# Optimization experiments

Measured on AMD Instinct MI355X. Metric: run time of the kernel, lower is better.

The kernel has to match this reference:

```python
import jax, jax.numpy as jnp
import numpy as np
from jax import lax

B, D, E, H, W = 256, 64, 16, 64, 64
PROJ, FC, NA = 512, 1024, 2

def _conv(x, w, pad):
    # x: [N,C,H,W], w: [O,I,kh,kw]
    return lax.conv_general_dilated(x, w, (1, 1), [(pad, pad), (pad, pad)],
                                    dimension_numbers=('NCHW', 'OIHW', 'NCHW'))

def _maxpool2(x):
    return lax.reduce_window(x, -jnp.inf, lax.max, (1, 1, 2, 2), (1, 1, 2, 2), 'VALID')

def _sample_conv(x, w, b):
    # per-sample conv with its own gathered expert weights: x [D,h,w], w [D,D,3,3]
    y = lax.conv_general_dilated(x[None], w, (1, 1), [(1, 1), (1, 1)],
                                 dimension_numbers=('NCHW', 'OIHW', 'NCHW'))[0]
    return y + b[:, None, None]

_expert_conv = jax.vmap(_sample_conv)  # batch of samples, each with its own kernel

def setup_inputs() -> dict:
    key = jax.random.key(0)
    ks = jax.random.split(key, 12)
    s = 0.05
    return {
        'image': jax.random.normal(ks[0], (B, 3, H, W), jnp.float32),
        'question': jax.random.randint(ks[1], (B, 8), 0, E),
        'stem_w0': jax.random.normal(ks[2], (D, 3, 3, 3), jnp.float32) * s,
        'stem_b0': jnp.zeros((D,), jnp.float32),
        'stem_w': jax.random.normal(ks[3], (3, D, D, 3, 3), jnp.float32) * s,
        'stem_b': jnp.zeros((3, D), jnp.float32),
        'exp_w1': jax.random.normal(ks[4], (E, D, D, 3, 3), jnp.float32) * s,
        'exp_b1': jnp.zeros((E, D), jnp.float32),
        'exp_w2': jax.random.normal(ks[5], (E, D, D, 3, 3), jnp.float32) * s,
        'exp_b2': jnp.zeros((E, D), jnp.float32),
        'proj_w': jax.random.normal(ks[6], (PROJ, D, 1, 1), jnp.float32) * s,
        'proj_b': jnp.zeros((PROJ,), jnp.float32),
        'fc1_w': jax.random.normal(ks[7], (FC, PROJ * 8 * 8), jnp.float32) * 0.01,
        'fc1_b': jnp.zeros((FC,), jnp.float32),
        'fc2_w': jax.random.normal(ks[8], (NA, FC), jnp.float32) * 0.01,
        'fc2_b': jnp.zeros((NA,), jnp.float32),
    }

def reference(image, question, stem_w0, stem_b0, stem_w, stem_b,
              exp_w1, exp_b1, exp_w2, exp_b2,
              proj_w, proj_b, fc1_w, fc1_b, fc2_w, fc2_b):
    # --- stem: 4 conv3x3 + ReLU, maxpool after layers 0 and 2 (64->32->16) ---
    h = jax.nn.relu(_conv(image, stem_w0, 1) + stem_b0[None, :, None, None])
    h = _maxpool2(h)
    h = jax.nn.relu(_conv(h, stem_w[0], 1) + stem_b[0][None, :, None, None])
    h = jax.nn.relu(_conv(h, stem_w[1], 1) + stem_b[1][None, :, None, None])
    h = _maxpool2(h)
    h = jax.nn.relu(_conv(h, stem_w[2], 1) + stem_b[2][None, :, None, None])
    # --- chain1 routing: cols (lhs=4, rel=5, rhs=7) each pick a ResidualBlock expert ---
    for col in (4, 5, 7):
        idx = question[:, col]                       # [B] expert ids
        w1, b1 = exp_w1[idx], exp_b1[idx]            # gather per-sample kernels
        w2, b2 = exp_w2[idx], exp_b2[idx]
        mid = jax.nn.relu(_expert_conv(h, w1, b1))   # conv1 + ReLU
        out = _expert_conv(mid, w2, b2)              # conv2 (no BN)
        h = jax.nn.relu(h + out)                     # residual + ReLU
    # --- classifier: 1x1 proj + ReLU, maxpool2, flatten, fc, fc ---
    c = jax.nn.relu(_conv(h, proj_w, 0) + proj_b[None, :, None, None])  # [B,512,16,16]
    c = _maxpool2(c)                                                     # [B,512,8,8]
    c = c.reshape(c.shape[0], -1)                                        # [B,32768]
    c = jax.nn.relu(c @ fc1_w.T + fc1_b)
    return c @ fc2_w.T + fc2_b                                           # [B,2]
```

## Files before the change

### kernel.cpp

```cpp
#include <hip/hip_runtime.h>
#include <cstddef>


typedef _Float16 half8 __attribute__((ext_vector_type(8)));
typedef _Float16 half4_t __attribute__((ext_vector_type(4)));
typedef float f32x4 __attribute__((ext_vector_type(4)));

#define LO_SCALE 2048.0f
#define LO_INV (1.0f / 2048.0f)

__global__ void transw_k(const float* __restrict__ src, float* __restrict__ dst,
                         int O, int I, int K, int total) {
    int id = blockIdx.x * 256 + threadIdx.x;
    if (id >= total) return;
    int OIK = O * I * K;
    int n = id / OIK, rem = id % OIK;
    int o = rem / (I * K), r2 = rem % (I * K);
    int i = r2 / K, k = r2 % K;
    dst[(size_t)n * OIK + (i * K + k) * O + o] = src[id];
}

__global__ void wxform_k(const float* __restrict__ src, _Float16* __restrict__ dst,
                         int nlayers) {
    int id = blockIdx.x * 256 + threadIdx.x;
    if (id >= nlayers * 36864) return;
    int layer = id / 36864, idx = id % 36864;
    int j = idx & 7, l = (idx >> 3) & 63, nt = (idx >> 9) & 3;
    int icc = (idx >> 11) & 1, tap = idx >> 12;
    int kl = (l >> 4) * 8 + j, ic = icc * 32 + kl, oc = nt * 16 + (l & 15);
    float v = src[(size_t)layer * 36864 + (oc * 64 + ic) * 9 + tap];
    _Float16 hi = (_Float16)v;
    _Float16 lo = (_Float16)((v - (float)hi) * LO_SCALE);
    dst[(size_t)layer * 73728 + idx] = hi;
    dst[(size_t)layer * 73728 + 36864 + idx] = lo;
}

__global__ void pwxform_k(const float* __restrict__ src, _Float16* __restrict__ dst) {
    int id = blockIdx.x * 256 + threadIdx.x;
    if (id >= 32768) return;
    int j = id & 7, l = (id >> 3) & 63, icc = (id >> 9) & 1, nt = id >> 10;
    int kl = (l >> 4) * 8 + j, ic = icc * 32 + kl, oc = nt * 16 + (l & 15);
    float v = src[oc * 64 + ic];
    _Float16 hi = (_Float16)v;
    _Float16 lo = (_Float16)((v - (float)hi) * LO_SCALE);
    dst[id] = hi;
    dst[32768 + id] = lo;
}

__global__ __launch_bounds__(256)
void conv1_k(const float* __restrict__ img, const float* __restrict__ w0t,
             const float* __restrict__ b0, float* __restrict__ out) {
    int b = blockIdx.x, tile = blockIdx.y, ocg = blockIdx.z;
    int typ = (tile >> 1) * 16, txp = (tile & 1) * 16;
    int cy0 = typ * 2, cx0 = txp * 2;
    __shared__ float lds[3][34][34];
    const float* imb = img + (size_t)b * 3 * 64 * 64;
    for (int i = threadIdx.x; i < 3 * 34 * 34; i += 256) {
        int c = i / 1156, rem = i % 1156, r = rem / 34, cc = rem % 34;
        int gy = cy0 - 1 + r, gx = cx0 - 1 + cc;
        float v = 0.f;
        if (gy >= 0 && gy < 64 && gx >= 0 && gx < 64) v = imb[(c * 64 + gy) * 64 + gx];
        lds[c][r][cc] = v;
    }
    __syncthreads();
    int pyl = threadIdx.x >> 4, pxl = threadIdx.x & 15;
    float win[3][4][4];
#pragma unroll
    for (int c = 0; c < 3; ++c)
#pragma unroll
        for (int wy = 0; wy < 4; ++wy)
#pragma unroll
            for (int wx = 0; wx < 4; ++wx)
                win[c][wy][wx] = lds[c][2 * pyl + wy][2 * pxl + wx];
    int py = typ + pyl, px = txp + pxl;
    float* op = &out[(((size_t)b * 32 + py) * 32 + px) * 64];
#pragma unroll
    for (int q = 0; q < 4; ++q) {
        int ocq = ocg * 4 + q;
        float acc[4][4] = {};
#pragma unroll
        for (int c = 0; c < 3; ++c)
#pragma unroll
            for (int ky = 0; ky < 3; ++ky)
#pragma unroll
                for (int kx = 0; kx < 3; ++kx) {
                    float4 w = *(const float4*)&w0t[(c * 9 + ky * 3 + kx) * 64 + ocq * 4];
                    float wv4[4] = {w.x, w.y, w.z, w.w};
#pragma unroll
                    for (int p2 = 0; p2 < 4; ++p2) {
                        float iv = win[c][(p2 >> 1) + ky][(p2 & 1) + kx];
#pragma unroll
                        for (int o = 0; o < 4; ++o)
                            acc[p2][o] = fmaf(iv, wv4[o], acc[p2][o]);
                    }
                }
        float4 res;
        float* rp = (float*)&res;
#pragma unroll
        for (int o = 0; o < 4; ++o) {
            float bvv = b0[ocq * 4 + o];
            float m = fmaxf(fmaxf(acc[0][o], acc[1][o]), fmaxf(acc[2][o], acc[3][o]));
            rp[o] = fmaxf(m + bvv, 0.f);
        }
        *(float4*)&op[ocq * 4] = res;
    }
}

template <int S, bool POOL, bool RES>
__global__ __launch_bounds__(256, 2)
void convm_k(const float* __restrict__ in, float* __restrict__ out,
             const _Float16* __restrict__ wf, const float* __restrict__ bias,
             const float* __restrict__ res, const int* __restrict__ question,
             int qcol) {
    int b = blockIdx.x, t = blockIdx.y;
    constexpr int NTX = S / 16;
    int ty0 = (t / NTX) * 8, tx0 = (t % NTX) * 16;

    __shared__ __align__(16) _Float16 lds[2 * 7200];

    int tid = threadIdx.x, lane = tid & 63, wv = tid >> 6;
    const _Float16* wb = wf;
    const float* bb = bias;
    if (question) {
        int idx = question[b * 8 + qcol];
        wb += (size_t)idx * 73728;
        bb += idx * 64;
    }
    float bv[4];
#pragma unroll
    for (int nt = 0; nt < 4; ++nt) bv[nt] = bb[nt * 16 + (lane & 15)];

    f32x4 acc1[2][4] = {};
    f32x4 acc2[2][4] = {};

    int am = lane & 15;
    int k0 = (lane >> 4) * 8;

    for (int icc = 0; icc < 2; ++icc) {
        __syncthreads();
        for (int i = tid; i < 1440; i += 256) {
            int pix = i >> 3, j4 = i & 7;
            int hy = pix / 18, hx = pix % 18;
            int gy = ty0 + hy - 1, gx = tx0 + hx - 1;
            float4 v = {0.f, 0.f, 0.f, 0.f};
            if (gy >= 0 && gy < S && gx >= 0 && gx < S)
                v = *(const float4*)&in[(((size_t)b * S + gy) * S + gx) * 64 + icc * 32 + j4 * 4];
            _Float16 h0 = (_Float16)v.x, h1 = (_Float16)v.y;
            _Float16 h2 = (_Float16)v.z, h3 = (_Float16)v.w;
            half4_t hh = {h0, h1, h2, h3};
            half4_t ll = {(_Float16)((v.x - (float)h0) * LO_SCALE),
                          (_Float16)((v.y - (float)h1) * LO_SCALE),
                          (_Float16)((v.z - (float)h2) * LO_SCALE),
                          (_Float16)((v.w - (float)h3) * LO_SCALE)};
            *(half4_t*)&lds[pix * 40 + j4 * 4] = hh;
            *(half4_t*)&lds[7200 + pix * 40 + j4 * 4] = ll;
        }
        __syncthreads();

#pragma unroll
        for (int ky = 0; ky < 3; ++ky)
#pragma unroll
            for (int kx = 0; kx < 3; ++kx) {
                int tap = ky * 3 + kx;
                const _Float16* wp = wb + (tap * 2 + icc) * 2048 + lane * 8;
                half8 bhi[4], blo[4];
#pragma unroll
                for (int nt = 0; nt < 4; ++nt) {
                    bhi[nt] = *(const half8*)(wp + nt * 512);
                    blo[nt] = *(const half8*)(wp + nt * 512 + 36864);
                }
#pragma unroll
                for (int mt = 0; mt < 2; ++mt) {
                    int MT = wv * 2 + mt;
                    int Q = MT * 4 + (am >> 2), s = am & 3;
                    int py = (Q >> 3) * 2 + (s >> 1), px = (Q & 7) * 2 + (s & 1);
                    const _Float16* ap = &lds[((py + ky) * 18 + (px + kx)) * 40 + k0];
                    half8 ahi = *(const half8*)ap;
                    half8 alo = *(const half8*)(ap + 7200);
#pragma unroll
                    for (int nt = 0; nt < 4; ++nt) {
                        acc1[mt][nt] = __builtin_amdgcn_mfma_f32_16x16x32_f16(
                            ahi, bhi[nt], acc1[mt][nt], 0, 0, 0);
                        acc2[mt][nt] = __builtin_amdgcn_mfma_f32_16x16x32_f16(
                            ahi, blo[nt], acc2[mt][nt], 0, 0, 0);
                        acc2[mt][nt] = __builtin_amdgcn_mfma_f32_16x16x32_f16(
                            alo, bhi[nt], acc2[mt][nt], 0, 0, 0);
                    }
                }
            }
    }

    int cn = lane & 15, rq = lane >> 4;
#pragma unroll
    for (int mt = 0; mt < 2; ++mt) {
        int MT = wv * 2 + mt;
        int Q = MT * 4 + rq;
        int qy = Q >> 3, qx = Q & 7;
#pragma unroll
        for (int nt = 0; nt < 4; ++nt) {
            int oc = nt * 16 + cn;
            float vals[4];
#pragma unroll
            for (int r = 0; r < 4; ++r)
                vals[r] = acc1[mt][nt][r] + acc2[mt][nt][r] * LO_INV + bv[nt];
            if (POOL) {
                float m = fmaxf(fmaxf(vals[0], vals[1]), fmaxf(vals[2], vals[3]));
                m = fmaxf(m, 0.f);
                int opy = (ty0 >> 1) + qy, opx = (tx0 >> 1) + qx;
                out[(((size_t)b * (S / 2) + opy) * (S / 2) + opx) * 64 + oc] = m;
            } else {
#pragma unroll
                for (int r = 0; r < 4; ++r) {
                    int py = qy * 2 + (r >> 1), px = qx * 2 + (r & 1);
                    size_t o = (((size_t)b * S + (ty0 + py)) * S + (tx0 + px)) * 64 + oc;
                    float v = vals[r];
                    if (RES) v += res[o];
                    out[o] = fmaxf(v, 0.f);
                }
            }
        }
    }
}

__global__ __launch_bounds__(256)
void projm_k(const float* __restrict__ in ,
             const _Float16* __restrict__ pw, const float* __restrict__ bias,
             float* __restrict__ out ) {
    int b = blockIdx.x;
    __shared__ float lt[64 * 65];
    int tid = threadIdx.x, lane = tid & 63, wv = tid >> 6;
    int row = lane & 15, cseg = lane >> 4;

    half8 ah[4][2], al[4][2];
#pragma unroll
    for (int mt = 0; mt < 4; ++mt) {
        int MT = wv * 4 + mt;
        int Q = MT * 4 + (row >> 2), s = row & 3;
        int y = (Q >> 3) * 2 + (s >> 1), x = (Q & 7) * 2 + (s & 1);
        const float* ip = in + ((size_t)b * 256 + y * 16 + x) * 64 + cseg * 8;
#pragma unroll
        for (int icc = 0; icc < 2; ++icc) {
            float4 v0 = *(const float4*)(ip + icc * 32);
            float4 v1 = *(const float4*)(ip + icc * 32 + 4);
            _Float16 h0 = (_Float16)v0.x, h1 = (_Float16)v0.y;
            _Float16 h2 = (_Float16)v0.z, h3 = (_Float16)v0.w;
            _Float16 h4 = (_Float16)v1.x, h5 = (_Float16)v1.y;
            _Float16 h6 = (_Float16)v1.z, h7 = (_Float16)v1.w;
            ah[mt][icc] = (half8){h0, h1, h2, h3, h4, h5, h6, h7};
            al[mt][icc] = (half8){(_Float16)((v0.x - (float)h0) * LO_SCALE),
                                  (_Float16)((v0.y - (float)h1) * LO_SCALE),
                                  (_Float16)((v0.z - (float)h2) * LO_SCALE),
                                  (_Float16)((v0.w - (float)h3) * LO_SCALE),
                                  (_Float16)((v1.x - (float)h4) * LO_SCALE),
                                  (_Float16)((v1.y - (float)h5) * LO_SCALE),
                                  (_Float16)((v1.z - (float)h6) * LO_SCALE),
                                  (_Float16)((v1.w - (float)h7) * LO_SCALE)};
        }
    }

    for (int ogl = 0; ogl < 4; ++ogl) {
        int og = blockIdx.y * 4 + ogl;
        half8 bh[4][2], bl[4][2];
#pragma unroll
        for (int ntl = 0; ntl < 4; ++ntl)
#pragma unroll
            for (int icc = 0; icc < 2; ++icc) {
                int nt = og * 4 + ntl;
                const _Float16* wp = pw + ((nt * 2 + icc) * 64 + lane) * 8;
                bh[ntl][icc] = *(const half8*)wp;
                bl[ntl][icc] = *(const half8*)(wp + 32768);
            }
        f32x4 a1[4][4] = {};
        f32x4 a2[4][4] = {};
#pragma unroll
        for (int icc = 0; icc < 2; ++icc)
#pragma unroll
            for (int mt = 0; mt < 4; ++mt)
#pragma unroll
                for (int ntl = 0; ntl < 4; ++ntl) {
                    a1[mt][ntl] = __builtin_amdgcn_mfma_f32_16x16x32_f16(
                        ah[mt][icc], bh[ntl][icc], a1[mt][ntl], 0, 0, 0);
                    a2[mt][ntl] = __builtin_amdgcn_mfma_f32_16x16x32_f16(
                        ah[mt][icc], bl[ntl][icc], a2[mt][ntl], 0, 0, 0);
                    a2[mt][ntl] = __builtin_amdgcn_mfma_f32_16x16x32_f16(
                        al[mt][icc], bh[ntl][icc], a2[mt][ntl], 0, 0, 0);
                }
        if (ogl) __syncthreads();
#pragma unroll
        for (int mt = 0; mt < 4; ++mt) {
            int Qg = (wv * 4 + mt) * 4 + (lane >> 4);
#pragma unroll
            for (int ntl = 0; ntl < 4; ++ntl) {
                float bvv = bias[og * 64 + ntl * 16 + (lane & 15)];
                float v0 = a1[mt][ntl][0] + a2[mt][ntl][0] * LO_INV + bvv;
                float v1 = a1[mt][ntl][1] + a2[mt][ntl][1] * LO_INV + bvv;
                float v2 = a1[mt][ntl][2] + a2[mt][ntl][2] * LO_INV + bvv;
                float v3 = a1[mt][ntl][3] + a2[mt][ntl][3] * LO_INV + bvv;
                float m = fmaxf(fmaxf(fmaxf(v0, v1), fmaxf(v2, v3)), 0.f);
                lt[(ntl * 16 + (lane & 15)) * 65 + Qg] = m;
            }
        }
        __syncthreads();
#pragma unroll
        for (int r = 0; r < 16; ++r) {
            int f = r * 256 + tid;
            int ol = f >> 6, q = f & 63;
            out[(size_t)b * 32768 + og * 4096 + ol * 64 + q] = lt[ol * 65 + q];
        }
    }
}

__global__ __launch_bounds__(256)
void fc1m_k(const float* __restrict__ A, const float* __restrict__ W,
            float* __restrict__ partial ) {
    int bid = blockIdx.x;
    int lid = (bid & 7) * 64 + (bid >> 3);
    int mt = lid & 1, nt = (lid >> 1) & 7, ks = lid >> 4;
    int m0 = mt * 128, n0 = nt * 128;
    const float* Ab = A + (size_t)m0 * 32768 + ks * 1024;
    const float* Wb = W + (size_t)n0 * 32768 + ks * 1024;

    __shared__ __align__(16) _Float16 lds[20480];
    _Float16* sa = lds;
    _Float16* sb = lds + 10240;

    int tid = threadIdx.x, lane = tid & 63, wv = tid >> 6;
    int wm = (wv & 1) * 64, wn = (wv >> 1) * 64;

    f32x4 acc1[4][4] = {};
    f32x4 acc2[4][4] = {};

    int row[4], c4[4];
#pragma unroll
    for (int p = 0; p < 4; ++p) {
        int idx = p * 256 + tid;
        row[p] = idx >> 3;
        c4[p] = (idx & 7) << 2;
    }

    float4 ra[4], rw[4];
#pragma unroll
    for (int p = 0; p < 4; ++p) {
        ra[p] = *(const float4*)&Ab[(size_t)row[p] * 32768 + c4[p]];
        rw[p] = *(const float4*)&Wb[(size_t)row[p] * 32768 + c4[p]];
    }

    for (int kt = 0; kt < 32; ++kt) {
#pragma unroll
        for (int p = 0; p < 4; ++p) {
            float4 v = ra[p];
            _Float16 h0 = (_Float16)v.x, h1 = (_Float16)v.y;
            _Float16 h2 = (_Float16)v.z, h3 = (_Float16)v.w;
            half4_t hh = {h0, h1, h2, h3};
            half4_t ll = {(_Float16)((v.x - (float)h0) * LO_SCALE),
                          (_Float16)((v.y - (float)h1) * LO_SCALE),
                          (_Float16)((v.z - (float)h2) * LO_SCALE),
                          (_Float16)((v.w - (float)h3) * LO_SCALE)};
            *(half4_t*)&sa[row[p] * 40 + c4[p]] = hh;
            *(half4_t*)&sa[5120 + row[p] * 40 + c4[p]] = ll;
            float4 u = rw[p];
            _Float16 g0 = (_Float16)u.x, g1 = (_Float16)u.y;
            _Float16 g2 = (_Float16)u.z, g3 = (_Float16)u.w;
            half4_t gh = {g0, g1, g2, g3};
            half4_t gl = {(_Float16)((u.x - (float)g0) * LO_SCALE),
                          (_Float16)((u.y - (float)g1) * LO_SCALE),
                          (_Float16)((u.z - (float)g2) * LO_SCALE),
                          (_Float16)((u.w - (float)g3) * LO_SCALE)};
            *(half4_t*)&sb[row[p] * 40 + c4[p]] = gh;
            *(half4_t*)&sb[5120 + row[p] * 40 + c4[p]] = gl;
        }
        __syncthreads();
        if (kt < 31) {
            int kb = (kt + 1) * 32;
#pragma unroll
            for (int p = 0; p < 4; ++p) {
                ra[p] = *(const float4*)&Ab[(size_t)row[p] * 32768 + kb + c4[p]];
                rw[p] = *(const float4*)&Wb[(size_t)row[p] * 32768 + kb + c4[p]];
            }
        }
        int koff = (lane >> 4) * 8;
        int fr = lane & 15;
        half8 bh[4], bl[4];
#pragma unroll
        for (int nf = 0; nf < 4; ++nf) {
            int r = wn + nf * 16 + fr;
            bh[nf] = *(const half8*)&sb[r * 40 + koff];
            bl[nf] = *(const half8*)&sb[5120 + r * 40 + koff];
        }
#pragma unroll
        for (int mf = 0; mf < 4; ++mf) {
            int r = wm + mf * 16 + fr;
            half8 ah = *(const half8*)&sa[r * 40 + koff];
            half8 al = *(const half8*)&sa[5120 + r * 40 + koff];
#pragma unroll
            for (int nf = 0; nf < 4; ++nf) {
                acc1[mf][nf] = __builtin_amdgcn_mfma_f32_16x16x32_f16(
                    ah, bh[nf], acc1[mf][nf], 0, 0, 0);
                acc2[mf][nf] = __builtin_amdgcn_mfma_f32_16x16x32_f16(
                    ah, bl[nf], acc2[mf][nf], 0, 0, 0);
                acc2[mf][nf] = __builtin_amdgcn_mfma_f32_16x16x32_f16(
                    al, bh[nf], acc2[mf][nf], 0, 0, 0);
            }
        }
        __syncthreads();
    }

    int rq = lane >> 4, cn = lane & 15;
    float* pb = partial + (size_t)ks * 262144;
#pragma unroll
    for (int mf = 0; mf < 4; ++mf)
#pragma unroll
        for (int nf = 0; nf < 4; ++nf) {
            int n = n0 + wn + nf * 16 + cn;
#pragma unroll
            for (int r = 0; r < 4; ++r) {
                int m = m0 + wm + mf * 16 + rq * 4 + r;
                pb[(size_t)m * 1024 + n] = acc1[mf][nf][r] + acc2[mf][nf][r] * LO_INV;
            }
        }
}

__global__ __launch_bounds__(256)
void fc1red_k(const float* __restrict__ partial, const float* __restrict__ b1,
              float* __restrict__ fc1o_t ) {
    int m = blockIdx.x;
    int n0 = threadIdx.x * 4;
    float4 s = {0.f, 0.f, 0.f, 0.f};
    for (int ks = 0; ks < 32; ++ks) {
        float4 v = *(const float4*)&partial[((size_t)ks * 256 + m) * 1024 + n0];
        s.x += v.x; s.y += v.y; s.z += v.z; s.w += v.w;
    }
    fc1o_t[(size_t)(n0 + 0) * 256 + m] = fmaxf(s.x + b1[n0 + 0], 0.f);
    fc1o_t[(size_t)(n0 + 1) * 256 + m] = fmaxf(s.y + b1[n0 + 1], 0.f);
    fc1o_t[(size_t)(n0 + 2) * 256 + m] = fmaxf(s.z + b1[n0 + 2], 0.f);
    fc1o_t[(size_t)(n0 + 3) * 256 + m] = fmaxf(s.w + b1[n0 + 3], 0.f);
}

__global__ __launch_bounds__(256)
void fc2a_k(const float* __restrict__ a_t, const float* __restrict__ W2,
            float* __restrict__ p2) {
    int n2 = blockIdx.x, ks = blockIdx.y;
    int m = threadIdx.x;
    float acc = 0.f;
    for (int k = ks * 256; k < ks * 256 + 256; ++k)
        acc = fmaf(a_t[(size_t)k * 256 + m], W2[n2 * 1024 + k], acc);
    p2[((size_t)n2 * 4 + ks) * 256 + m] = acc;
}

__global__ __launch_bounds__(512)
void fc2b_k(const float* __restrict__ p2, const float* __restrict__ b2,
            float* __restrict__ out) {
    int i = threadIdx.x;
    int m = i >> 1, n2 = i & 1;
    float s = b2[n2];
#pragma unroll
    for (int ks = 0; ks < 4; ++ks) s += p2[((size_t)n2 * 4 + ks) * 256 + m];
    out[m * 2 + n2] = s;
}

extern "C" void kernel_launch(void* const* d_in, const int* in_sizes, int n_in,
                              void* d_out, int out_size, void* d_ws, size_t ws_size,
                              hipStream_t stream) {
    const float* image   = (const float*)d_in[0];
    const int*   question= (const int*)d_in[1];
    const float* stem_w0 = (const float*)d_in[2];
    const float* stem_b0 = (const float*)d_in[3];
    const float* stem_w  = (const float*)d_in[4];
    const float* stem_b  = (const float*)d_in[5];
    const float* exp_w1  = (const float*)d_in[6];
    const float* exp_b1  = (const float*)d_in[7];
    const float* exp_w2  = (const float*)d_in[8];
    const float* exp_b2  = (const float*)d_in[9];
    const float* proj_w  = (const float*)d_in[10];
    const float* proj_b  = (const float*)d_in[11];
    const float* fc1_w   = (const float*)d_in[12];
    const float* fc1_b   = (const float*)d_in[13];
    const float* fc2_w   = (const float*)d_in[14];
    const float* fc2_b   = (const float*)d_in[15];
    (void)in_sizes; (void)n_in; (void)out_size; (void)ws_size;

    float* ws = (float*)d_ws;
    const size_t A = 16777216, P2N = 4194304;
    float* p1    = ws;
    float* h2    = ws + A;
    float* p2    = ws + 2 * A;
    float* wtr   = ws + 2 * A + P2N;
    float* w0t   = wtr;
    _Float16* pwF = (_Float16*)(wtr + 1728);
    float* pfc2  = wtr + 1728 + 32768;
    _Float16* f16b = (_Float16*)(wtr + 36544);
    _Float16* stemtF = f16b;
    _Float16* e1tF   = f16b + 3 * 73728;
    _Float16* e2tF   = e1tF + 16 * 73728;
    float* hA    = ws;
    float* hB    = ws + P2N;
    float* hC    = ws + 2 * P2N;
    float* pool3 = h2;
    float* fc1o  = h2 + 8388608;
    float* fc1p  = ws;

    transw_k<<<(1728 + 255) / 256, 256, 0, stream>>>(stem_w0, w0t, 64, 3, 9, 1728);
    pwxform_k<<<128, 256, 0, stream>>>(proj_w, pwF);
    wxform_k<<<(3 * 36864 + 255) / 256, 256, 0, stream>>>(stem_w, stemtF, 3);
    wxform_k<<<(16 * 36864 + 255) / 256, 256, 0, stream>>>(exp_w1, e1tF, 16);
    wxform_k<<<(16 * 36864 + 255) / 256, 256, 0, stream>>>(exp_w2, e2tF, 16);

    conv1_k<<<dim3(256, 4, 4), 256, 0, stream>>>(image, w0t, stem_b0, p1);
    convm_k<32, false, false><<<dim3(256, 8), 256, 0, stream>>>(
        p1, h2, stemtF, stem_b, nullptr, nullptr, 0);
    convm_k<32, true, false><<<dim3(256, 8), 256, 0, stream>>>(
        h2, p2, stemtF + 73728, stem_b + 64, nullptr, nullptr, 0);
    convm_k<16, false, false><<<dim3(256, 2), 256, 0, stream>>>(
        p2, hA, stemtF + 2 * 73728, stem_b + 128, nullptr, nullptr, 0);

    const int cols[3] = {4, 5, 7};
    float* hin = hA;
    float* hmid = hB;
    float* hout = hC;
    for (int r = 0; r < 3; ++r) {
        convm_k<16, false, false><<<dim3(256, 2), 256, 0, stream>>>(
            hin, hmid, e1tF, exp_b1, nullptr, question, cols[r]);
        convm_k<16, false, true><<<dim3(256, 2), 256, 0, stream>>>(
            hmid, hout, e2tF, exp_b2, hin, question, cols[r]);
        float* tp = hin; hin = hout; hout = hmid; hmid = tp;
    }

    projm_k<<<dim3(256, 2), 256, 0, stream>>>(hin, pwF, proj_b, pool3);
    fc1m_k<<<512, 256, 0, stream>>>(pool3, fc1_w, fc1p);
    fc1red_k<<<256, 256, 0, stream>>>(fc1p, fc1_b, fc1o);
    fc2a_k<<<dim3(2, 4), 256, 0, stream>>>(fc1o, fc2_w, pfc2);
    fc2b_k<<<1, 512, 0, stream>>>(pfc2, fc2_b, (float*)d_out);
}
```

Baseline: 463.9 us.

## Pre-split fc1 activations to fp16 hi/lo in projection and double split-K

The projection kernel now writes its pooled output directly as fp16 high and scaled-low halves, so the fc1 GEMM loads ready-made half8 vectors instead of converting fp32 activations in its inner loop. fc1 split-K goes from 32 to 64 slices, giving 1024 blocks with a 4-blocks-per-CU launch bound for more parallelism, and the reduction now sums 64 partials. The tradeoff is a partial-sum buffer twice as large, which adds write and read traffic in the reduction.

After: 894.4 us. 92.8% more time.

```diff
diff --git a/kernel.cpp b/kernel.cpp
--- a/kernel.cpp
+++ b/kernel.cpp
@@ -225,7 +225,7 @@
 __global__ __launch_bounds__(256)
 void projm_k(const float* __restrict__ in ,
              const _Float16* __restrict__ pw, const float* __restrict__ bias,
-             float* __restrict__ out ) {
+             _Float16* __restrict__ outh ) {
     int b = blockIdx.x;
     __shared__ float lt[64 * 65];
     int tid = threadIdx.x, lane = tid & 63, wv = tid >> 6;
@@ -305,20 +305,26 @@
         for (int r = 0; r < 16; ++r) {
             int f = r * 256 + tid;
             int ol = f >> 6, q = f & 63;
-            out[(size_t)b * 32768 + og * 4096 + ol * 64 + q] = lt[ol * 65 + q];
-        }
-    }
-}
-
-__global__ __launch_bounds__(256)
-void fc1m_k(const float* __restrict__ A, const float* __restrict__ W,
+            float v = lt[ol * 65 + q];
+            _Float16 h = (_Float16)v;
+            _Float16 l = (_Float16)((v - (float)h) * LO_SCALE);
+            size_t o = (size_t)b * 32768 + og * 4096 + ol * 64 + q;
+            outh[o] = h;
+            outh[8388608 + o] = l;
+        }
+    }
+}
+
+__global__ __launch_bounds__(256, 4)
+void fc1m_k(const _Float16* __restrict__ Ahl ,
+            const float* __restrict__ W,
             float* __restrict__ partial ) {
     int bid = blockIdx.x;
-    int lid = (bid & 7) * 64 + (bid >> 3);
+    int lid = (bid & 7) * 128 + (bid >> 3);
     int mt = lid & 1, nt = (lid >> 1) & 7, ks = lid >> 4;
     int m0 = mt * 128, n0 = nt * 128;
-    const float* Ab = A + (size_t)m0 * 32768 + ks * 1024;
-    const float* Wb = W + (size_t)n0 * 32768 + ks * 1024;
+    const _Float16* Ab = Ahl + (size_t)m0 * 32768 + ks * 512;
+    const float* Wb = W + (size_t)n0 * 32768 + ks * 512;
 
     __shared__ __align__(16) _Float16 lds[20480];
     _Float16* sa = lds;
@@ -330,34 +336,40 @@
     f32x4 acc1[4][4] = {};
     f32x4 acc2[4][4] = {};
 
-    int row[4], c4[4];
+    int arow[2], ak8[2];
+#pragma unroll
+    for (int p = 0; p < 2; ++p) {
+        int idx = p * 256 + tid;
+        arow[p] = idx >> 2;
+        ak8[p] = (idx & 3) * 8;
+    }
+    int wrow[4], wc4[4];
 #pragma unroll
     for (int p = 0; p < 4; ++p) {
         int idx = p * 256 + tid;
-        row[p] = idx >> 3;
-        c4[p] = (idx & 7) << 2;
-    }
-
-    float4 ra[4], rw[4];
-#pragma unroll
-    for (int p = 0; p < 4; ++p) {
-        ra[p] = *(const float4*)&Ab[(size_t)row[p] * 32768 + c4[p]];
-        rw[p] = *(const float4*)&Wb[(size_t)row[p] * 32768 + c4[p]];
-    }
-
-    for (int kt = 0; kt < 32; ++kt) {
+        wrow[p] = idx >> 3;
+        wc4[p] = (idx & 7) << 2;
+    }
+
+    half8 pa_h[2], pa_l[2];
+    float4 rw[4];
+#pragma unroll
+    for (int p = 0; p < 2; ++p) {
+        pa_h[p] = *(const half8*)&Ab[(size_t)arow[p] * 32768 + ak8[p]];
+        pa_l[p] = *(const half8*)&Ab[8388608 + (size_t)arow[p] * 32768 + ak8[p]];
+    }
+#pragma unroll
+    for (int p = 0; p < 4; ++p)
+        rw[p] = *(const float4*)&Wb[(size_t)wrow[p] * 32768 + wc4[p]];
+
+    for (int kt = 0; kt < 16; ++kt) {
+#pragma unroll
+        for (int p = 0; p < 2; ++p) {
+            *(half8*)&sa[arow[p] * 40 + ak8[p]] = pa_h[p];
+            *(half8*)&sa[5120 + arow[p] * 40 + ak8[p]] = pa_l[p];
+        }
 #pragma unroll
         for (int p = 0; p < 4; ++p) {
-            float4 v = ra[p];
-            _Float16 h0 = (_Float16)v.x, h1 = (_Float16)v.y;
-            _Float16 h2 = (_Float16)v.z, h3 = (_Float16)v.w;
-            half4_t hh = {h0, h1, h2, h3};
-            half4_t ll = {(_Float16)((v.x - (float)h0) * LO_SCALE),
-                          (_Float16)((v.y - (float)h1) * LO_SCALE),
-                          (_Float16)((v.z - (float)h2) * LO_SCALE),
-                          (_Float16)((v.w - (float)h3) * LO_SCALE)};
-            *(half4_t*)&sa[row[p] * 40 + c4[p]] = hh;
-            *(half4_t*)&sa[5120 + row[p] * 40 + c4[p]] = ll;
             float4 u = rw[p];
             _Float16 g0 = (_Float16)u.x, g1 = (_Float16)u.y;
             _Float16 g2 = (_Float16)u.z, g3 = (_Float16)u.w;
@@ -366,17 +378,20 @@
                           (_Float16)((u.y - (float)g1) * LO_SCALE),
                           (_Float16)((u.z - (float)g2) * LO_SCALE),
                           (_Float16)((u.w - (float)g3) * LO_SCALE)};
-            *(half4_t*)&sb[row[p] * 40 + c4[p]] = gh;
-            *(half4_t*)&sb[5120 + row[p] * 40 + c4[p]] = gl;
+            *(half4_t*)&sb[wrow[p] * 40 + wc4[p]] = gh;
+            *(half4_t*)&sb[5120 + wrow[p] * 40 + wc4[p]] = gl;
         }
         __syncthreads();
-        if (kt < 31) {
+        if (kt < 15) {
             int kb = (kt + 1) * 32;
 #pragma unroll
-            for (int p = 0; p < 4; ++p) {
-                ra[p] = *(const float4*)&Ab[(size_t)row[p] * 32768 + kb + c4[p]];
-                rw[p] = *(const float4*)&Wb[(size_t)row[p] * 32768 + kb + c4[p]];
-            }
+            for (int p = 0; p < 2; ++p) {
+                pa_h[p] = *(const half8*)&Ab[(size_t)arow[p] * 32768 + kb + ak8[p]];
+                pa_l[p] = *(const half8*)&Ab[8388608 + (size_t)arow[p] * 32768 + kb + ak8[p]];
+            }
+#pragma unroll
+            for (int p = 0; p < 4; ++p)
+                rw[p] = *(const float4*)&Wb[(size_t)wrow[p] * 32768 + kb + wc4[p]];
         }
         int koff = (lane >> 4) * 8;
         int fr = lane & 15;
@@ -426,7 +441,7 @@
     int m = blockIdx.x;
     int n0 = threadIdx.x * 4;
     float4 s = {0.f, 0.f, 0.f, 0.f};
-    for (int ks = 0; ks < 32; ++ks) {
+    for (int ks = 0; ks < 64; ++ks) {
         float4 v = *(const float4*)&partial[((size_t)ks * 256 + m) * 1024 + n0];
         s.x += v.x; s.y += v.y; s.z += v.z; s.w += v.w;
     }
@@ -495,7 +510,7 @@
     float* hA    = ws;
     float* hB    = ws + P2N;
     float* hC    = ws + 2 * P2N;
-    float* pool3 = h2;
+    _Float16* pool3h = (_Float16*)h2;
     float* fc1o  = h2 + 8388608;
     float* fc1p  = ws;
 
@@ -525,8 +540,8 @@
         float* tp = hin; hin = hout; hout = hmid; hmid = tp;
     }
 
-    projm_k<<<dim3(256, 2), 256, 0, stream>>>(hin, pwF, proj_b, pool3);
-    fc1m_k<<<512, 256, 0, stream>>>(pool3, fc1_w, fc1p);
+    projm_k<<<dim3(256, 2), 256, 0, stream>>>(hin, pwF, proj_b, pool3h);
+    fc1m_k<<<1024, 256, 0, stream>>>(pool3h, fc1_w, fc1p);
     fc1red_k<<<256, 256, 0, stream>>>(fc1p, fc1_b, fc1o);
     fc2a_k<<<dim3(2, 4), 256, 0, stream>>>(fc1o, fc2_w, pfc2);
     fc2b_k<<<1, 512, 0, stream>>>(pfc2, fc2_b, (float*)d_out);
```
